# Kernel optimization log

Measured on AMD Instinct MI355X. Metric: run time of the kernel, lower is better.

## Reference

```python
import jax, jax.numpy as jnp
import numpy as np

SCALE = 1.0  # Scaler(scale=1.0) is a fixed multiplicative scale


def setup_inputs() -> dict:
    key = jax.random.key(0)
    ks = jax.random.split(key, 7)
    d = 2048          # in_features == out_features (per-head proj dim)
    out_total = 3 * d # fused QKV weight rows
    r = 8             # LoRA rank
    B, S = 4, 2048
    return {
        "x": jax.random.normal(ks[0], (B, S, d), dtype=jnp.float32),
        "W": jax.random.normal(ks[1], (out_total, d), dtype=jnp.float32) * 0.02,
        "b": jax.random.normal(ks[2], (out_total,), dtype=jnp.float32) * 0.02,
        "A1": jax.random.normal(ks[3], (r, d), dtype=jnp.float32) * 0.02,
        "B1": jax.random.normal(ks[4], (d, r), dtype=jnp.float32) * 0.02,
        "A2": jax.random.normal(ks[5], (r, d), dtype=jnp.float32) * 0.02,
        "B2": jax.random.normal(ks[6], (d, r), dtype=jnp.float32) * 0.02,
    }


def reference(x, W, b, A1, B1, A2, B2):
    # Low-rank deltas for K and V rows: each [out_features, in_features]
    dK = SCALE * (B1 @ A1)            # [d, d]
    dV = SCALE * (B2 @ A2)            # [d, d]
    delta = jnp.concatenate([dK, dV], axis=0)          # [2d, d]
    # zero-pad on top to match full fused weight (Q rows untouched)
    pad_rows = W.shape[0] - delta.shape[0]
    delta_full = jnp.concatenate(
        [jnp.zeros((pad_rows, W.shape[1]), dtype=W.dtype), delta], axis=0
    )                                                    # [3d, d]
    weight = W + delta_full
    # F.linear: x @ weight.T + b
    return jnp.einsum("bsd,od->bso", x, weight) + b
```

## Files before the change

kernel.cpp:

```cpp
#include <hip/hip_runtime.h>
#include <hip/hip_bf16.h>
#include <stdint.h>
#include <stddef.h>

typedef __attribute__((ext_vector_type(8)))  __bf16 bf16x8;
typedef __attribute__((ext_vector_type(16))) float  f32x16;
typedef __attribute__((ext_vector_type(8)))  unsigned short ushort8;

typedef const void __attribute__((address_space(1)))* as1_cvp;
typedef void       __attribute__((address_space(3)))* as3_vp;

__device__ __forceinline__ void gload_lds16(const void* g, void* l) {
    __builtin_amdgcn_global_load_lds((as1_cvp)g, (as3_vp)l, 16, 0, 0);
}

__device__ __forceinline__ unsigned short f2bf(float f) {
    union { float f; unsigned u; } v; v.f = f;
    unsigned r = v.u + 0x7fffu + ((v.u >> 16) & 1u);
    return (unsigned short)(r >> 16);
}

__global__ __launch_bounds__(256) void prep_kernel(
    const float* __restrict__ x,
    const float* __restrict__ W,
    const float* __restrict__ A1, const float* __restrict__ B1,
    const float* __restrict__ A2, const float* __restrict__ B2,
    unsigned short* __restrict__ Xb, unsigned short* __restrict__ Wb,
    int d, int nW, int n8)
{
    int blk = blockIdx.x;
    if (blk < nW) {
        int o  = blk;
        int k0 = threadIdx.x * 8;
        const float4* wrow = (const float4*)(W + (size_t)o * d + k0);
        float4 w0 = wrow[0], w1 = wrow[1];
        float acc[8] = {w0.x, w0.y, w0.z, w0.w, w1.x, w1.y, w1.z, w1.w};
        if (o >= d) {
            const float* A  = (o < 2 * d) ? A1 : A2;
            const float* Bm = (o < 2 * d) ? B1 : B2;
            int r0 = o - ((o < 2 * d) ? d : 2 * d);
#pragma unroll
            for (int r = 0; r < 8; ++r) {
                float bb = Bm[(size_t)r0 * 8 + r];
                const float4* arow = (const float4*)(A + (size_t)r * d + k0);
                float4 a0 = arow[0], a1 = arow[1];
                acc[0] += bb * a0.x; acc[1] += bb * a0.y;
                acc[2] += bb * a0.z; acc[3] += bb * a0.w;
                acc[4] += bb * a1.x; acc[5] += bb * a1.y;
                acc[6] += bb * a1.z; acc[7] += bb * a1.w;
            }
        }
        ushort8 ov;
#pragma unroll
        for (int c = 0; c < 8; ++c) ov[c] = f2bf(acc[c]);
        ((ushort8*)(Wb + (size_t)o * d))[threadIdx.x] = ov;
    } else {
        int i = (blk - nW) * 256 + threadIdx.x;
        if (i >= n8) return;
        const float4* s = (const float4*)x + (size_t)i * 2;
        float4 a = s[0], c = s[1];
        ushort8 o;
        o[0] = f2bf(a.x); o[1] = f2bf(a.y); o[2] = f2bf(a.z); o[3] = f2bf(a.w);
        o[4] = f2bf(c.x); o[5] = f2bf(c.y); o[6] = f2bf(c.z); o[7] = f2bf(c.w);
        ((ushort8*)Xb)[i] = o;
    }
}

constexpr int BM = 256, BN = 256, BK = 64;
constexpr int KK = 2048, NN = 6144;
constexpr int TT = KK / BK;

__global__ __launch_bounds__(512, 2) void gemm256_kernel(
    const unsigned short* __restrict__ Xb,
    const unsigned short* __restrict__ Wb,
    const float* __restrict__ bias,
    float* __restrict__ out,
    int M)
{
    __shared__ __align__(16) unsigned short As[2][BM * BK];
    __shared__ __align__(16) unsigned short Bs[2][BN * BK];

    const int tid  = threadIdx.x;
    const int wave = tid >> 6;
    const int lane = tid & 63;
    const int half = lane >> 5;
    const int ln32 = lane & 31;
    const int wrow = wave >> 2;
    const int wcol = wave & 3;

    int nwg = (int)gridDim.x;
    int bid = (int)blockIdx.x;
    int swz = bid;
    if ((nwg & 7) == 0) swz = (bid & 7) * (nwg >> 3) + (bid >> 3);
    const int ntn = NN / BN;
    const int bm = (swz / ntn) * BM;
    const int bn = (swz % ntn) * BN;

    const int rtid = tid >> 3;
    const int ctid = (tid & 7) ^ (rtid & 7);
    const size_t gA0 = (size_t)(bm + rtid) * KK + ctid * 8;
    const size_t gB0 = (size_t)(bn + rtid) * KK + ctid * 8;
    const int ldsW = wave * 512;

#define STAGE_A(t, j, buf) gload_lds16(Xb + gA0 + (size_t)(j) * 64 * KK + (size_t)(t) * BK, \
                                       &As[(buf)][(j) * 4096 + ldsW])
#define STAGE_B(t, j, buf) gload_lds16(Wb + gB0 + (size_t)(j) * 64 * KK + (size_t)(t) * BK, \
                                       &Bs[(buf)][(j) * 4096 + ldsW])

    const int r7 = ln32 & 7;
    int dofs[4];
#pragma unroll
    for (int s = 0; s < 4; ++s) dofs[s] = ((s * 2 + half) ^ r7) * 8;
    int baseA[2][2];
#pragma unroll
    for (int qm = 0; qm < 2; ++qm)
#pragma unroll
        for (int f = 0; f < 2; ++f)
            baseA[qm][f] = (wrow * 128 + qm * 64 + f * 32 + ln32) * BK;
    int baseB[2];
#pragma unroll
    for (int qn = 0; qn < 2; ++qn) baseB[qn] = (wcol * 64 + qn * 32 + ln32) * BK;

    f32x16 acc[4][2];
#pragma unroll
    for (int i = 0; i < 4; ++i)
#pragma unroll
        for (int j = 0; j < 2; ++j)
#pragma unroll
            for (int r = 0; r < 16; ++r) acc[i][j][r] = 0.f;

    bf16x8 a[2][4], b0[4], b1[4];

#define LOAD_A(qm) do { _Pragma("unroll") for (int s = 0; s < 4; ++s) {        \
        a[0][s] = *(const bf16x8*)&Aq[baseA[qm][0] + dofs[s]];                 \
        a[1][s] = *(const bf16x8*)&Aq[baseA[qm][1] + dofs[s]]; } } while (0)
#define LOAD_B(qn, BB) do { _Pragma("unroll") for (int s = 0; s < 4; ++s) {    \
        BB[s] = *(const bf16x8*)&Bq[baseB[qn] + dofs[s]]; } } while (0)
#define MFMA_CL(i0, i1, jj, BB) do {                                           \
        __builtin_amdgcn_s_setprio(1);                                         \
        _Pragma("unroll") for (int s = 0; s < 4; ++s) {                        \
            acc[i0][jj] = __builtin_amdgcn_mfma_f32_32x32x16_bf16(a[0][s], BB[s], acc[i0][jj], 0, 0, 0); \
            acc[i1][jj] = __builtin_amdgcn_mfma_f32_32x32x16_bf16(a[1][s], BB[s], acc[i1][jj], 0, 0, 0); \
        }                                                                      \
        __builtin_amdgcn_s_setprio(0); } while (0)
#define BAR() asm volatile("s_barrier" ::: "memory")

#define GROUP(v, SN1, SN2, VMW) do {                                           \
        const int q_ = (v) & 1;                                                \
        const unsigned short* Aq = &As[q_][0];                                 \
        const unsigned short* Bq = &Bs[q_][0];                                 \
                                                                      \
        LOAD_A(0); LOAD_B(0, b0);                                              \
        if (SN1) { STAGE_B((v) + 1, 2, q_ ^ 1); STAGE_B((v) + 1, 3, q_ ^ 1); } \
        BAR();                                                                 \
        MFMA_CL(0, 1, 0, b0);                                                  \
        BAR();                                                                 \
                                                                      \
        LOAD_B(1, b1);                                                         \
        if (SN1) { STAGE_A((v) + 1, 1, q_ ^ 1); STAGE_A((v) + 1, 3, q_ ^ 1); } \
        BAR();                                                                 \
        MFMA_CL(0, 1, 1, b1);                                                  \
        BAR();                                                                 \
                                                                      \
        LOAD_A(1);                                                             \
        if (SN2) { STAGE_A((v) + 2, 0, q_); STAGE_A((v) + 2, 2, q_); }         \
        BAR();                                                                 \
        MFMA_CL(2, 3, 0, b0);                                                  \
        BAR();                                                                 \
                                                                      \
        if (SN2) { STAGE_B((v) + 2, 0, q_); STAGE_B((v) + 2, 1, q_); }         \
        if ((VMW) == 4)      asm volatile("s_waitcnt vmcnt(4)" ::: "memory");  \
        else if ((VMW) == 0) asm volatile("s_waitcnt vmcnt(0)" ::: "memory");  \
        BAR();                                                                 \
        MFMA_CL(2, 3, 1, b1);                                                  \
        BAR();                                                                 \
    } while (0)

#pragma unroll
    for (int j = 0; j < 4; ++j) STAGE_A(0, j, 0);
#pragma unroll
    for (int j = 0; j < 4; ++j) STAGE_B(0, j, 0);
    STAGE_A(1, 0, 1); STAGE_A(1, 2, 1);
    STAGE_B(1, 0, 1); STAGE_B(1, 1, 1);
    asm volatile("s_waitcnt vmcnt(4)" ::: "memory");
    BAR();

#pragma unroll 2
    for (int v = 0; v < TT - 2; ++v) GROUP(v, 1, 1, 4);
    GROUP(TT - 2, 1, 0, 0);
    GROUP(TT - 1, 0, 0, -1);

#undef GROUP
#undef BAR
#undef MFMA_CL
#undef LOAD_B
#undef LOAD_A
#undef STAGE_B
#undef STAGE_A

#pragma unroll
    for (int j = 0; j < 2; ++j) {
        int col = bn + wcol * 64 + j * 32 + ln32;
        float bv = bias[col];
#pragma unroll
        for (int i = 0; i < 4; ++i) {
            int rbase = bm + wrow * 128 + i * 32 + 4 * half;
#pragma unroll
            for (int reg = 0; reg < 16; ++reg) {
                int row = rbase + (reg & 3) + 8 * (reg >> 2);
                out[(size_t)row * NN + col] = acc[i][j][reg] + bv;
            }
        }
    }
}

extern "C" void kernel_launch(void* const* d_in, const int* in_sizes, int n_in,
                              void* d_out, int out_size, void* d_ws, size_t ws_size,
                              hipStream_t stream) {
    const float* x  = (const float*)d_in[0];
    const float* W  = (const float*)d_in[1];
    const float* b  = (const float*)d_in[2];
    const float* A1 = (const float*)d_in[3];
    const float* B1 = (const float*)d_in[4];
    const float* A2 = (const float*)d_in[5];
    const float* B2 = (const float*)d_in[6];
    float* out = (float*)d_out;

    const int d = 2048;
    const int K = d;
    const int N = 3 * d;
    const int M = in_sizes[0] / d;

    unsigned short* Xbf = (unsigned short*)d_ws;
    unsigned short* Wbf = Xbf + (size_t)M * K;

    int n8 = (M * K) / 8;
    int castBlocks = (n8 + 255) / 256;
    prep_kernel<<<N + castBlocks, 256, 0, stream>>>(x, W, A1, B1, A2, B2,
                                                    Xbf, Wbf, d, N, n8);

    dim3 grid((M / BM) * (N / BN));
    gemm256_kernel<<<grid, 512, 0, stream>>>(Xbf, Wbf, b, out, M);
}
```

Before: 484.7 us.

## Prefetch next tile's LDS fragments during last MFMA cluster of each group

Splits the A register fragments into two double-buffered sets and moves the LDS reads for the next k-tile's first A/B fragments into the final MFMA phase of the current group, so LDS read latency overlaps matrix math. The buffer parity becomes a compile-time constant by manually unrolling the loop in pairs. This costs more VGPRs for the extra fragment set, which may lower occupancy or cause spills. It also assumes TT is even.

```diff
diff --git a/kernel.cpp b/kernel.cpp
--- a/kernel.cpp
+++ b/kernel.cpp
@@ -129,51 +129,52 @@
 #pragma unroll
             for (int r = 0; r < 16; ++r) acc[i][j][r] = 0.f;
 
-    bf16x8 a[2][4], b0[4], b1[4];
-
-#define LOAD_A(qm) do { _Pragma("unroll") for (int s = 0; s < 4; ++s) {        \
-        a[0][s] = *(const bf16x8*)&Aq[baseA[qm][0] + dofs[s]];                 \
-        a[1][s] = *(const bf16x8*)&Aq[baseA[qm][1] + dofs[s]]; } } while (0)
-#define LOAD_B(qn, BB) do { _Pragma("unroll") for (int s = 0; s < 4; ++s) {    \
-        BB[s] = *(const bf16x8*)&Bq[baseB[qn] + dofs[s]]; } } while (0)
-#define MFMA_CL(i0, i1, jj, BB) do {                                           \
-        __builtin_amdgcn_s_setprio(1);                                         \
-        _Pragma("unroll") for (int s = 0; s < 4; ++s) {                        \
-            acc[i0][jj] = __builtin_amdgcn_mfma_f32_32x32x16_bf16(a[0][s], BB[s], acc[i0][jj], 0, 0, 0); \
-            acc[i1][jj] = __builtin_amdgcn_mfma_f32_32x32x16_bf16(a[1][s], BB[s], acc[i1][jj], 0, 0, 0); \
-        }                                                                      \
+    bf16x8 a0f[2][4], a1f[2][4], b0[4], b1[4];
+
+#define LOAD_AQ(SRC, qm, DST) do { _Pragma("unroll") for (int s = 0; s < 4; ++s) {  \
+        DST[0][s] = *(const bf16x8*)&(SRC)[baseA[qm][0] + dofs[s]];                 \
+        DST[1][s] = *(const bf16x8*)&(SRC)[baseA[qm][1] + dofs[s]]; } } while (0)
+#define LOAD_BQ(SRC, qn, DST) do { _Pragma("unroll") for (int s = 0; s < 4; ++s) {  \
+        DST[s] = *(const bf16x8*)&(SRC)[baseB[qn] + dofs[s]]; } } while (0)
+#define MFMA_CL(AF, i0, i1, jj, BB) do {                                            \
+        __builtin_amdgcn_s_setprio(1);                                             \
+        _Pragma("unroll") for (int s = 0; s < 4; ++s) {                            \
+            acc[i0][jj] = __builtin_amdgcn_mfma_f32_32x32x16_bf16(AF[0][s], BB[s], acc[i0][jj], 0, 0, 0); \
+            acc[i1][jj] = __builtin_amdgcn_mfma_f32_32x32x16_bf16(AF[1][s], BB[s], acc[i1][jj], 0, 0, 0); \
+        }                                                                          \
         __builtin_amdgcn_s_setprio(0); } while (0)
 #define BAR() asm volatile("s_barrier" ::: "memory")
 
-#define GROUP(v, SN1, SN2, VMW) do {                                           \
-        const int q_ = (v) & 1;                                                \
-        const unsigned short* Aq = &As[q_][0];                                 \
-        const unsigned short* Bq = &Bs[q_][0];                                 \
-                                                                      \
-        LOAD_A(0); LOAD_B(0, b0);                                              \
-        if (SN1) { STAGE_B((v) + 1, 2, q_ ^ 1); STAGE_B((v) + 1, 3, q_ ^ 1); } \
-        BAR();                                                                 \
-        MFMA_CL(0, 1, 0, b0);                                                  \
-        BAR();                                                                 \
-                                                                      \
-        LOAD_B(1, b1);                                                         \
-        if (SN1) { STAGE_A((v) + 1, 1, q_ ^ 1); STAGE_A((v) + 1, 3, q_ ^ 1); } \
-        BAR();                                                                 \
-        MFMA_CL(0, 1, 1, b1);                                                  \
-        BAR();                                                                 \
-                                                                      \
-        LOAD_A(1);                                                             \
-        if (SN2) { STAGE_A((v) + 2, 0, q_); STAGE_A((v) + 2, 2, q_); }         \
-        BAR();                                                                 \
-        MFMA_CL(2, 3, 0, b0);                                                  \
-        BAR();                                                                 \
-                                                                      \
-        if (SN2) { STAGE_B((v) + 2, 0, q_); STAGE_B((v) + 2, 1, q_); }         \
-        if ((VMW) == 4)      asm volatile("s_waitcnt vmcnt(4)" ::: "memory");  \
-        else if ((VMW) == 0) asm volatile("s_waitcnt vmcnt(0)" ::: "memory");  \
-        BAR();                                                                 \
-        MFMA_CL(2, 3, 1, b1);                                                  \
-        BAR();                                                                 \
+#define GROUP(v, QQ, SN1, SN2, VMW, RN) do {                                       \
+        const unsigned short* Aq  = &As[(QQ)][0];                                  \
+        const unsigned short* Bq  = &Bs[(QQ)][0];                                  \
+        const unsigned short* Aq2 = &As[(QQ) ^ 1][0];                              \
+        const unsigned short* Bq2 = &Bs[(QQ) ^ 1][0];                              \
+                  \
+        LOAD_BQ(Bq, 1, b1);                                                        \
+        if (SN1) { STAGE_B((v) + 1, 2, (QQ) ^ 1); STAGE_B((v) + 1, 3, (QQ) ^ 1); } \
+        BAR();                                                                     \
+        MFMA_CL(a0f, 0, 1, 0, b0);                                                 \
+        BAR();                                                                     \
+                                       \
+        LOAD_AQ(Aq, 1, a1f);                                                       \
+        if (SN1) { STAGE_A((v) + 1, 1, (QQ) ^ 1); STAGE_A((v) + 1, 3, (QQ) ^ 1); } \
+        BAR();                                                                     \
+        MFMA_CL(a0f, 0, 1, 1, b1);                                                 \
+        BAR();                                                                     \
+                                                       \
+        if (SN2) { STAGE_A((v) + 2, 0, (QQ)); STAGE_A((v) + 2, 2, (QQ)); }         \
+        BAR();                                                                     \
+        MFMA_CL(a1f, 2, 3, 0, b0);                                                 \
+        BAR();                                                                     \
+               \
+        if (SN2) { STAGE_B((v) + 2, 0, (QQ)); STAGE_B((v) + 2, 1, (QQ)); }         \
+        if ((VMW) == 4)      asm volatile("s_waitcnt vmcnt(4)" ::: "memory");      \
+        else if ((VMW) == 0) asm volatile("s_waitcnt vmcnt(0)" ::: "memory");      \
+        BAR();                                                                     \
+        if (RN) { LOAD_AQ(Aq2, 0, a0f); LOAD_BQ(Bq2, 0, b0); }                     \
+        MFMA_CL(a1f, 2, 3, 1, b1);                                                 \
+        BAR();                                                                     \
     } while (0)
 
 #pragma unroll
@@ -184,17 +185,21 @@
     STAGE_B(1, 0, 1); STAGE_B(1, 1, 1);
     asm volatile("s_waitcnt vmcnt(4)" ::: "memory");
     BAR();
-
-#pragma unroll 2
-    for (int v = 0; v < TT - 2; ++v) GROUP(v, 1, 1, 4);
-    GROUP(TT - 2, 1, 0, 0);
-    GROUP(TT - 1, 0, 0, -1);
+    LOAD_AQ((&As[0][0]), 0, a0f);
+    LOAD_BQ((&Bs[0][0]), 0, b0);
+
+    for (int vv = 0; vv < TT - 2; vv += 2) {
+        GROUP(vv,     0, 1, 1, 4, 1);
+        GROUP(vv + 1, 1, 1, 1, 4, 1);
+    }
+    GROUP(TT - 2, 0, 1, 0, 0, 1);
+    GROUP(TT - 1, 1, 0, 0, -1, 0);
 
 #undef GROUP
 #undef BAR
 #undef MFMA_CL
-#undef LOAD_B
-#undef LOAD_A
+#undef LOAD_BQ
+#undef LOAD_AQ
 #undef STAGE_B
 #undef STAGE_A
 
```

After: 531.2 us. 9.6% more time.
